# Kernel tuning notes

Measured on AMD Instinct MI355X. Metric: run time of the kernel, lower is better.

## Reference

```python
import jax, jax.numpy as jnp
import numpy as np

EMBED = 768
HEAD = 256

def setup_inputs() -> dict:
    key = jax.random.key(0)
    k1, k2, k3, k4 = jax.random.split(key, 4)
    res_stream = jax.random.normal(k1, (512, 128, EMBED), dtype=jnp.float32)
    # torch Linear(embed, head, bias=False): y = x @ W.T, W: [head, embed].
    # Store as [embed, head] so y = x @ W.
    Wk = jax.random.normal(k2, (EMBED, HEAD), dtype=jnp.float32) * (EMBED ** -0.5)
    Wq = jax.random.normal(k3, (EMBED, HEAD), dtype=jnp.float32) * (EMBED ** -0.5)
    Wv = jax.random.normal(k4, (EMBED, HEAD), dtype=jnp.float32) * (EMBED ** -0.5)
    return {"res_stream": res_stream, "Wk": Wk, "Wq": Wq, "Wv": Wv}

def reference(res_stream, Wk, Wq, Wv):
    B, T, E = res_stream.shape
    q = jnp.einsum('bte,eh->bth', res_stream, Wq)  # [B,T,H]
    k = jnp.einsum('bte,eh->bth', res_stream, Wk)
    v = jnp.einsum('bte,eh->bth', res_stream, Wv)
    # NOTE: original scales by embed**-0.5 (not head_size**-0.5)
    scores = jnp.einsum('bth,bsh->bts', q, k) * (E ** -0.5)  # [B,T,T]
    causal = jnp.tril(jnp.ones((T, T), dtype=bool))
    scores = jnp.where(causal, scores, -jnp.inf)
    attn = jax.nn.softmax(scores, axis=-1)
    # dropout: eval mode (identity) for deterministic reference
    return jnp.einsum('bts,bsh->bth', attn, v)  # [B,T,H]
```

## Files before the change

kernel.cpp:

```cpp
#include <hip/hip_runtime.h>
#include <hip/hip_bf16.h>

typedef float f32x4 __attribute__((ext_vector_type(4)));
typedef short bfx8 __attribute__((ext_vector_type(8)));

typedef const __attribute__((address_space(1))) void* gvp;
typedef __attribute__((address_space(3))) void* lvp;

static __device__ __forceinline__ unsigned short f2bf(float f) {
    return __builtin_bit_cast(unsigned short, __float2bfloat16(f));
}

static __device__ __forceinline__ bfx8 cvt8(f32x4 lo, f32x4 hi) {
    bfx8 r;
    r[0] = (short)f2bf(lo[0]); r[1] = (short)f2bf(lo[1]);
    r[2] = (short)f2bf(lo[2]); r[3] = (short)f2bf(lo[3]);
    r[4] = (short)f2bf(hi[0]); r[5] = (short)f2bf(hi[1]);
    r[6] = (short)f2bf(hi[2]); r[7] = (short)f2bf(hi[3]);
    return r;
}

__global__ void prep_w(const float* __restrict__ Wk, const float* __restrict__ Wq,
                       const float* __restrict__ Wv, unsigned short* __restrict__ WT) {
    const int n = blockIdx.x;
    const int e = threadIdx.x;
    const int which = n >> 8;
    const int h = n & 255;
    const float* W = (which == 0) ? Wq : (which == 1) ? Wk : Wv;
    WT[(size_t)n * 768 + e] = f2bf(W[(size_t)e * 256 + h]);
}

__global__ void cvt_x(const float* __restrict__ X, unsigned short* __restrict__ Xb,
                      long n) {
    long i = ((long)blockIdx.x * 256 + threadIdx.x) * 8;
    const long stride = (long)gridDim.x * 256 * 8;
    for (; i < n; i += stride) {
        f32x4 lo = *(const f32x4*)(X + i);
        f32x4 hi = *(const f32x4*)(X + i + 4);
        *(bfx8*)(Xb + i) = cvt8(lo, hi);
    }
}

__global__ __launch_bounds__(256) void qkv_gemm(const unsigned short* __restrict__ Xb,
                                                const unsigned short* __restrict__ WT,
                                                unsigned short* __restrict__ QKV,
                                                int b0, int nwg) {
    __shared__ __align__(16) char LDS[65536];

    const int tid = threadIdx.x;
    const int bid = blockIdx.x;
    const int q = nwg >> 3, r = nwg & 7;
    const int xcd = bid & 7, idx = bid >> 3;
    const int l = (xcd < r ? xcd * (q + 1) : r * (q + 1) + (xcd - r) * q) + idx;
    const int bn = l % 6;
    const int bm = l / 6;
    const int m0 = bm * 128;
    const int n0 = bn * 128;
    const int w = tid >> 6, lane = tid & 63;
    const int wr = w >> 1, wc = w & 1;
    const int lrow = lane & 15, lhi = lane >> 4;
    const bool vswap = (bn >= 4);

    f32x4 acc[4][4];
    const f32x4 zero = {0.f, 0.f, 0.f, 0.f};
#pragma unroll
    for (int i = 0; i < 4; ++i)
#pragma unroll
        for (int j = 0; j < 4; ++j) acc[i][j] = zero;

#define STAGE(kt, bs)                                                          \
    {                                                                          \
        const int k0s = (kt) * 64;                                             \
        _Pragma("unroll")                                                      \
        for (int i = 0; i < 4; ++i) {                                          \
            const int f = i * 256 + tid;                                       \
            const int row = f >> 3;                                            \
            const int cbs = ((f & 7) * 16) ^ ((row & 7) << 4);                 \
            const unsigned short* ga = Xb + (size_t)(m0 + row) * 768 + k0s + (cbs >> 1); \
            char* lpa = LDS + (bs) * 16384 + i * 4096 + w * 1024;              \
            __builtin_amdgcn_global_load_lds((gvp)ga, (lvp)lpa, 16, 0, 0);     \
            const unsigned short* gb = WT + (size_t)(n0 + row) * 768 + k0s + (cbs >> 1); \
            char* lpb = LDS + 32768 + (bs) * 16384 + i * 4096 + w * 1024;      \
            __builtin_amdgcn_global_load_lds((gvp)gb, (lvp)lpb, 16, 0, 0);     \
        }                                                                      \
    }

    STAGE(0, 0);
    STAGE(1, 1);

    int cur = 0;
    for (int kt = 0; kt < 12; ++kt) {
        if (kt < 11) asm volatile("s_waitcnt vmcnt(8)" ::: "memory");
        else         asm volatile("s_waitcnt vmcnt(0)" ::: "memory");
        __builtin_amdgcn_s_barrier();
#pragma unroll
        for (int kk = 0; kk < 2; ++kk) {
            const int kb2 = (kk * 32 + lhi * 8) * 2;
            bfx8 a[4], bb4[4];
#pragma unroll
            for (int mi = 0; mi < 4; ++mi) {
                const int arow = wr * 64 + mi * 16 + lrow;
                a[mi] = *(const bfx8*)(LDS + cur * 16384 + arow * 128 +
                                       (kb2 ^ ((arow & 7) << 4)));
            }
#pragma unroll
            for (int ni = 0; ni < 4; ++ni) {
                const int brow = wc * 64 + ni * 16 + lrow;
                bb4[ni] = *(const bfx8*)(LDS + 32768 + cur * 16384 + brow * 128 +
                                         (kb2 ^ ((brow & 7) << 4)));
            }
            if (!vswap) {
#pragma unroll
                for (int mi = 0; mi < 4; ++mi)
#pragma unroll
                    for (int ni = 0; ni < 4; ++ni)
                        acc[mi][ni] = __builtin_amdgcn_mfma_f32_16x16x32_bf16(
                            a[mi], bb4[ni], acc[mi][ni], 0, 0, 0);
            } else {
#pragma unroll
                for (int ni = 0; ni < 4; ++ni)
#pragma unroll
                    for (int mi = 0; mi < 4; ++mi)
                        acc[ni][mi] = __builtin_amdgcn_mfma_f32_16x16x32_bf16(
                            bb4[ni], a[mi], acc[ni][mi], 0, 0, 0);
            }
        }
        __builtin_amdgcn_s_barrier();
        if (kt < 10) STAGE(kt + 2, cur);
        cur ^= 1;
    }

    const int b = b0 + bm;
    if (!vswap) {
        const int which = bn >> 1;
        const size_t base = ((size_t)(b * 3 + which)) << 15;
        const int hbase = (bn & 1) * 128;
#pragma unroll
        for (int mi = 0; mi < 4; ++mi)
#pragma unroll
            for (int ni = 0; ni < 4; ++ni) {
                const int t = wr * 64 + mi * 16 + lhi * 4;
                const int h = hbase + wc * 64 + ni * 16 + lrow;
#pragma unroll
                for (int j = 0; j < 4; ++j)
                    QKV[base + (size_t)(t + j) * 256 + h] = f2bf(acc[mi][ni][j]);
            }
    } else {
        const size_t base = ((size_t)(b * 3 + 2)) << 15;
#pragma unroll
        for (int ni = 0; ni < 4; ++ni)
#pragma unroll
            for (int mi = 0; mi < 4; ++mi) {
                const int h = (bn - 4) * 128 + wc * 64 + ni * 16 + lhi * 4;
                const int t = wr * 64 + mi * 16 + lrow;
#pragma unroll
                for (int j = 0; j < 4; ++j)
                    QKV[base + (size_t)(h + j) * 128 + t] = f2bf(acc[ni][mi][j]);
            }
    }
}

__global__ __launch_bounds__(512) void attn(const unsigned short* __restrict__ QKV,
                                            float* __restrict__ Out) {
    __shared__ unsigned short Kl[128][264];
    __shared__ unsigned short Vt[256][136];

    const int b = blockIdx.x;
    const int tid = threadIdx.x;
    const int w = tid >> 6, lane = tid & 63;
    const int lrow = lane & 15, lhi = lane >> 4;

    const unsigned short* Qb = QKV + ((size_t)(b * 3 + 0) << 15);
    const unsigned short* Kb = QKV + ((size_t)(b * 3 + 1) << 15);
    const unsigned short* Vb = QKV + ((size_t)(b * 3 + 2) << 15);

    const int t0 = w * 16;
    bfx8 aq[8];
#pragma unroll
    for (int kk = 0; kk < 8; ++kk)
        aq[kk] = *(const bfx8*)(Qb + (size_t)(t0 + lrow) * 256 + kk * 32 + lhi * 8);

#pragma unroll
    for (int i = 0; i < 8; ++i) {
        int f = i * 512 + tid;
        {
            int row = f >> 5, c = (f & 31) * 8;
            *(bfx8*)&Kl[row][c] = *(const bfx8*)(Kb + (size_t)row * 256 + c);
        }
        {
            int row = f >> 4, c = (f & 15) * 8;
            *(bfx8*)&Vt[row][c] = *(const bfx8*)(Vb + (size_t)row * 128 + c);
        }
    }
    __syncthreads();

    f32x4 sacc[8];
    const f32x4 zero = {0.f, 0.f, 0.f, 0.f};
#pragma unroll
    for (int sj = 0; sj < 8; ++sj) sacc[sj] = zero;
#pragma unroll
    for (int kk = 0; kk < 8; ++kk) {
        const int kb = kk * 32 + lhi * 8;
#pragma unroll
        for (int sj = 0; sj < 8; ++sj) {
            bfx8 bk = *(const bfx8*)&Kl[sj * 16 + lrow][kb];
            sacc[sj] = __builtin_amdgcn_mfma_f32_16x16x32_bf16(aq[kk], bk, sacc[sj], 0, 0, 0);
        }
    }

    const float scale = 0.03608439182435161f;
    float inv[4];
#pragma unroll
    for (int j = 0; j < 4; ++j) {
        const int t = t0 + lhi * 4 + j;
        float m = -1e30f;
#pragma unroll
        for (int sj = 0; sj < 8; ++sj) {
            int s = sj * 16 + lrow;
            float vv = sacc[sj][j] * scale;
            vv = (s <= t) ? vv : -1e30f;
            sacc[sj][j] = vv;
            m = fmaxf(m, vv);
        }
#pragma unroll
        for (int d = 1; d < 16; d <<= 1) m = fmaxf(m, __shfl_xor(m, d));
        float sum = 0.f;
#pragma unroll
        for (int sj = 0; sj < 8; ++sj) {
            float e = __expf(sacc[sj][j] - m);
            sacc[sj][j] = e;
            sum += e;
        }
#pragma unroll
        for (int d = 1; d < 16; d <<= 1) sum += __shfl_xor(sum, d);
        inv[j] = 1.0f / sum;
    }

    __syncthreads();

    unsigned short* Pl = &Kl[0][0] + (size_t)w * (16 * 136);
#pragma unroll
    for (int sj = 0; sj < 8; ++sj)
#pragma unroll
        for (int j = 0; j < 4; ++j)
            Pl[(lhi * 4 + j) * 136 + sj * 16 + lrow] = f2bf(sacc[sj][j] * inv[j]);

    bfx8 pa[4];
#pragma unroll
    for (int kk = 0; kk < 4; ++kk)
        pa[kk] = *(const bfx8*)(Pl + lrow * 136 + kk * 32 + lhi * 8);

    f32x4 oacc[16];
#pragma unroll
    for (int ni = 0; ni < 16; ++ni) oacc[ni] = zero;
#pragma unroll
    for (int ni = 0; ni < 16; ++ni) {
#pragma unroll
        for (int kk = 0; kk < 4; ++kk) {
            bfx8 bv = *(const bfx8*)&Vt[ni * 16 + lrow][kk * 32 + lhi * 8];
            oacc[ni] = __builtin_amdgcn_mfma_f32_16x16x32_bf16(pa[kk], bv, oacc[ni], 0, 0, 0);
        }
    }

    float* Ob = Out + (size_t)b * 128 * 256;
#pragma unroll
    for (int ni = 0; ni < 16; ++ni) {
#pragma unroll
        for (int j = 0; j < 4; ++j) {
            const int t = t0 + lhi * 4 + j;
            const int h = ni * 16 + lrow;
            Ob[(size_t)t * 256 + h] = oacc[ni][j];
        }
    }
}

extern "C" void kernel_launch(void* const* d_in, const int* in_sizes, int n_in,
                              void* d_out, int out_size, void* d_ws, size_t ws_size,
                              hipStream_t stream) {
    (void)in_sizes; (void)n_in; (void)out_size;
    const float* X  = (const float*)d_in[0];
    const float* Wk = (const float*)d_in[1];
    const float* Wq = (const float*)d_in[2];
    const float* Wv = (const float*)d_in[3];

    const size_t WT_E  = (size_t)768 * 768;
    const size_t QKV_E = (size_t)512 * 3 * 32768;
    unsigned short* WT  = (unsigned short*)d_ws;
    unsigned short* QKV = WT + WT_E;
    unsigned short* Xb  = QKV + QKV_E;
    float* Out = (float*)d_out;

    const long perBatch = 128 * 768;
    size_t used = (WT_E + QKV_E) * 2;
    size_t availB = (ws_size > used) ? ws_size - used : 0;
    int chunk = (int)((availB / 2) / (size_t)perBatch);
    if (chunk > 512) chunk = 512;
    if (chunk < 1) chunk = 1;

    prep_w<<<768, 768, 0, stream>>>(Wk, Wq, Wv, WT);
    for (int b0 = 0; b0 < 512; b0 += chunk) {
        const int cb = (512 - b0 < chunk) ? (512 - b0) : chunk;
        const long n = (long)cb * perBatch;
        cvt_x<<<2048, 256, 0, stream>>>(X + (size_t)b0 * perBatch, Xb, n);
        const int nwg = cb * 6;
        qkv_gemm<<<nwg, 256, 0, stream>>>(Xb, WT, QKV, b0, nwg);
    }
    attn<<<512, 512, 0, stream>>>(QKV, Out);
}
```

Before: 198.9 us.

## Widen QKV GEMM tile to 128x256 with a K-step of 32

The QKV projection GEMM now uses 128x256 output tiles, so each workgroup produces a full Q, K or V head block, where before it produced a 128x128 half. The K step shrinks from 64 to 32 and the LDS swizzle is redone for 64-byte rows, which cuts LDS use to 48KB. The aim is to halve redundant loads of the X tile and halve the number of workgroups, so each one does more MFMA work per staged byte. In exchange, each thread holds twice as many accumulators, which may reduce occupancy, and the grid has half as many workgroups.

```diff
diff --git a/kernel.cpp b/kernel.cpp
--- a/kernel.cpp
+++ b/kernel.cpp
@@ -45,42 +45,48 @@
                                                 const unsigned short* __restrict__ WT,
                                                 unsigned short* __restrict__ QKV,
                                                 int b0, int nwg) {
-    __shared__ __align__(16) char LDS[65536];
+    __shared__ __align__(16) char LDS[49152];
 
     const int tid = threadIdx.x;
     const int bid = blockIdx.x;
     const int q = nwg >> 3, r = nwg & 7;
     const int xcd = bid & 7, idx = bid >> 3;
     const int l = (xcd < r ? xcd * (q + 1) : r * (q + 1) + (xcd - r) * q) + idx;
-    const int bn = l % 6;
-    const int bm = l / 6;
+    const int bn = l % 3;
+    const int bm = l / 3;
     const int m0 = bm * 128;
-    const int n0 = bn * 128;
+    const int n0 = bn * 256;
     const int w = tid >> 6, lane = tid & 63;
     const int wr = w >> 1, wc = w & 1;
     const int lrow = lane & 15, lhi = lane >> 4;
-    const bool vswap = (bn >= 4);
-
-    f32x4 acc[4][4];
+    const bool vswap = (bn == 2);
+
+    f32x4 acc[4][8];
     const f32x4 zero = {0.f, 0.f, 0.f, 0.f};
 #pragma unroll
     for (int i = 0; i < 4; ++i)
 #pragma unroll
-        for (int j = 0; j < 4; ++j) acc[i][j] = zero;
+        for (int j = 0; j < 8; ++j) acc[i][j] = zero;
 
 #define STAGE(kt, bs)                                                          \
     {                                                                          \
-        const int k0s = (kt) * 64;                                             \
+        const int k0s = (kt) * 32;                                             \
+        _Pragma("unroll")                                                      \
+        for (int i = 0; i < 2; ++i) {                                          \
+            const int f = i * 256 + tid;                                       \
+            const int row = f >> 2;                                            \
+            const int cbs = ((f & 3) * 16) ^ (((row >> 1) & 3) << 4);          \
+            const unsigned short* ga = Xb + (size_t)(m0 + row) * 768 + k0s + (cbs >> 1); \
+            char* lpa = LDS + (bs) * 8192 + i * 4096 + tid * 16;               \
+            __builtin_amdgcn_global_load_lds((gvp)ga, (lvp)lpa, 16, 0, 0);     \
+        }                                                                      \
         _Pragma("unroll")                                                      \
         for (int i = 0; i < 4; ++i) {                                          \
             const int f = i * 256 + tid;                                       \
-            const int row = f >> 3;                                            \
-            const int cbs = ((f & 7) * 16) ^ ((row & 7) << 4);                 \
-            const unsigned short* ga = Xb + (size_t)(m0 + row) * 768 + k0s + (cbs >> 1); \
-            char* lpa = LDS + (bs) * 16384 + i * 4096 + w * 1024;              \
-            __builtin_amdgcn_global_load_lds((gvp)ga, (lvp)lpa, 16, 0, 0);     \
+            const int row = f >> 2;                                            \
+            const int cbs = ((f & 3) * 16) ^ (((row >> 1) & 3) << 4);          \
             const unsigned short* gb = WT + (size_t)(n0 + row) * 768 + k0s + (cbs >> 1); \
-            char* lpb = LDS + 32768 + (bs) * 16384 + i * 4096 + w * 1024;      \
+            char* lpb = LDS + 16384 + (bs) * 16384 + i * 4096 + tid * 16;      \
             __builtin_amdgcn_global_load_lds((gvp)gb, (lvp)lpb, 16, 0, 0);     \
         }                                                                      \
     }
@@ -89,73 +95,69 @@
     STAGE(1, 1);
 
     int cur = 0;
-    for (int kt = 0; kt < 12; ++kt) {
-        if (kt < 11) asm volatile("s_waitcnt vmcnt(8)" ::: "memory");
+    for (int kt = 0; kt < 24; ++kt) {
+        if (kt < 23) asm volatile("s_waitcnt vmcnt(6)" ::: "memory");
         else         asm volatile("s_waitcnt vmcnt(0)" ::: "memory");
         __builtin_amdgcn_s_barrier();
-#pragma unroll
-        for (int kk = 0; kk < 2; ++kk) {
-            const int kb2 = (kk * 32 + lhi * 8) * 2;
-            bfx8 a[4], bb4[4];
+        {
+            const int cb = lhi * 16;
+            bfx8 a[4], bb4[8];
 #pragma unroll
             for (int mi = 0; mi < 4; ++mi) {
                 const int arow = wr * 64 + mi * 16 + lrow;
-                a[mi] = *(const bfx8*)(LDS + cur * 16384 + arow * 128 +
-                                       (kb2 ^ ((arow & 7) << 4)));
-            }
-#pragma unroll
-            for (int ni = 0; ni < 4; ++ni) {
-                const int brow = wc * 64 + ni * 16 + lrow;
-                bb4[ni] = *(const bfx8*)(LDS + 32768 + cur * 16384 + brow * 128 +
-                                         (kb2 ^ ((brow & 7) << 4)));
+                a[mi] = *(const bfx8*)(LDS + cur * 8192 + arow * 64 +
+                                       (cb ^ (((arow >> 1) & 3) << 4)));
+            }
+#pragma unroll
+            for (int ni = 0; ni < 8; ++ni) {
+                const int brow = wc * 128 + ni * 16 + lrow;
+                bb4[ni] = *(const bfx8*)(LDS + 16384 + cur * 16384 + brow * 64 +
+                                         (cb ^ (((brow >> 1) & 3) << 4)));
             }
             if (!vswap) {
 #pragma unroll
                 for (int mi = 0; mi < 4; ++mi)
 #pragma unroll
-                    for (int ni = 0; ni < 4; ++ni)
+                    for (int ni = 0; ni < 8; ++ni)
                         acc[mi][ni] = __builtin_amdgcn_mfma_f32_16x16x32_bf16(
                             a[mi], bb4[ni], acc[mi][ni], 0, 0, 0);
             } else {
 #pragma unroll
-                for (int ni = 0; ni < 4; ++ni)
-#pragma unroll
-                    for (int mi = 0; mi < 4; ++mi)
-                        acc[ni][mi] = __builtin_amdgcn_mfma_f32_16x16x32_bf16(
-                            bb4[ni], a[mi], acc[ni][mi], 0, 0, 0);
+                for (int mi = 0; mi < 4; ++mi)
+#pragma unroll
+                    for (int ni = 0; ni < 8; ++ni)
+                        acc[mi][ni] = __builtin_amdgcn_mfma_f32_16x16x32_bf16(
+                            bb4[ni], a[mi], acc[mi][ni], 0, 0, 0);
             }
         }
         __builtin_amdgcn_s_barrier();
-        if (kt < 10) STAGE(kt + 2, cur);
+        if (kt < 22) STAGE(kt + 2, cur);
         cur ^= 1;
     }
 
     const int b = b0 + bm;
+    const size_t base = ((size_t)(b * 3 + bn)) << 15;
     if (!vswap) {
-        const int which = bn >> 1;
-        const size_t base = ((size_t)(b * 3 + which)) << 15;
-        const int hbase = (bn & 1) * 128;
 #pragma unroll
         for (int mi = 0; mi < 4; ++mi)
 #pragma unroll
-            for (int ni = 0; ni < 4; ++ni) {
+            for (int ni = 0; ni < 8; ++ni) {
                 const int t = wr * 64 + mi * 16 + lhi * 4;
-                const int h = hbase + wc * 64 + ni * 16 + lrow;
+                const int h = wc * 128 + ni * 16 + lrow;
 #pragma unroll
                 for (int j = 0; j < 4; ++j)
                     QKV[base + (size_t)(t + j) * 256 + h] = f2bf(acc[mi][ni][j]);
             }
     } else {
-        const size_t base = ((size_t)(b * 3 + 2)) << 15;
-#pragma unroll
-        for (int ni = 0; ni < 4; ++ni)
-#pragma unroll
-            for (int mi = 0; mi < 4; ++mi) {
-                const int h = (bn - 4) * 128 + wc * 64 + ni * 16 + lhi * 4;
+#pragma unroll
+        for (int mi = 0; mi < 4; ++mi)
+#pragma unroll
+            for (int ni = 0; ni < 8; ++ni) {
+                const int h = wc * 128 + ni * 16 + lhi * 4;
                 const int t = wr * 64 + mi * 16 + lrow;
 #pragma unroll
                 for (int j = 0; j < 4; ++j)
-                    QKV[base + (size_t)(h + j) * 128 + t] = f2bf(acc[ni][mi][j]);
+                    QKV[base + (size_t)(h + j) * 128 + t] = f2bf(acc[mi][ni][j]);
             }
     }
 }
@@ -302,7 +304,7 @@
         const int cb = (512 - b0 < chunk) ? (512 - b0) : chunk;
         const long n = (long)cb * perBatch;
         cvt_x<<<2048, 256, 0, stream>>>(X + (size_t)b0 * perBatch, Xb, n);
-        const int nwg = cb * 6;
+        const int nwg = cb * 3;
         qkv_gemm<<<nwg, 256, 0, stream>>>(Xb, WT, QKV, b0, nwg);
     }
     attn<<<512, 512, 0, stream>>>(QKV, Out);
```

Result: slower. 226.3 us (+13.8%).
